# Optimization experiments

Measured on AMD Instinct MI355X. Metric: run time of the kernel, lower is better.

Reference implementation:

```python
import jax, jax.numpy as jnp
import numpy as np

B, H, W, C = 2, 192, 192, 192
WS, SHIFT, NH = 16, 8, 6


def _window_partition(x, ws):
    b, h, w, c = x.shape
    x = x.reshape(b, h // ws, ws, w // ws, ws, c)
    return x.transpose(0, 1, 3, 2, 4, 5).reshape(-1, ws, ws, c)


def _window_reverse(win, ws, h, w):
    b = win.shape[0] // ((h // ws) * (w // ws))
    x = win.reshape(b, h // ws, w // ws, ws, ws, -1)
    return x.transpose(0, 1, 3, 2, 4, 5).reshape(b, h, w, -1)


def _relative_position_index(ws):
    coords = np.stack(np.meshgrid(np.arange(ws), np.arange(ws), indexing="ij"))
    cf = coords.reshape(2, -1)
    rel = (cf[:, :, None] - cf[:, None, :]).transpose(1, 2, 0).astype(np.int64)
    rel[..., 0] += ws - 1
    rel[..., 1] += ws - 1
    rel[..., 0] *= 2 * ws - 1
    return rel.sum(-1)  # (ws*ws, ws*ws) in [0, (2ws-1)^2)


def _shift_attn_mask(h, w, ws, shift):
    img = np.zeros((1, h, w, 1), np.float32)
    cnt = 0
    for hs in (slice(0, -ws), slice(-ws, -shift), slice(-shift, None)):
        for wsl in (slice(0, -ws), slice(-ws, -shift), slice(-shift, None)):
            img[:, hs, wsl, :] = cnt
            cnt += 1
    mw = np.asarray(_window_partition(jnp.asarray(img), ws)).reshape(-1, ws * ws)
    diff = mw[:, None, :] - mw[:, :, None]
    return jnp.asarray(np.where(diff != 0, -100.0, 0.0).astype(np.float32))


def setup_inputs():
    key = jax.random.key(0)
    ks = jax.random.split(key, 4)
    x = jax.random.normal(ks[0], (B, H, W, C), jnp.float32)
    qkv = jax.random.normal(ks[1], (B, H, W, 3 * C), jnp.float32)
    rpb_table = 0.02 * jax.random.normal(ks[2], ((2 * WS - 1) ** 2, NH), jnp.float32)
    geo_scale = jnp.full((NH,), 0.01, jnp.float32)
    geo_sigma = jnp.asarray(1.0, jnp.float32)
    proj_w = 0.02 * jax.random.normal(ks[3], (C, C), jnp.float32)
    proj_b = jnp.zeros((C,), jnp.float32)
    rpi = jnp.asarray(_relative_position_index(WS), jnp.int32)
    attn_mask = _shift_attn_mask(H, W, WS, SHIFT)
    return dict(x=x, qkv=qkv, rpb_table=rpb_table, geo_scale=geo_scale,
                geo_sigma=geo_sigma, proj_w=proj_w, proj_b=proj_b,
                rpi=rpi, attn_mask=attn_mask,
                window_size=WS, shift_size=SHIFT, num_heads=NH)


def _geo_bias(f, ws, sigma):
    # f: (nwb, ws, ws, C). L-shaped geodesic path: horizontal then vertical cumsums.
    nwb = f.shape[0]
    diff_h = jnp.sum(jnp.abs(f[:, :, 1:] - f[:, :, :-1]), -1)  # (nwb, ws, ws-1)
    ct_h = jnp.cumsum(jnp.concatenate(
        [jnp.zeros((nwb, ws, 1), f.dtype), 1.0 + sigma * diff_h], -1), -1)
    diff_v = jnp.sum(jnp.abs(f[:, 1:] - f[:, :-1]), -1)        # (nwb, ws-1, ws)
    ct_v = jnp.cumsum(jnp.concatenate(
        [jnp.zeros((nwb, 1, ws), f.dtype), 1.0 + sigma * diff_v], -2), -2)
    idx = jnp.arange(ws * ws)
    rows, cols = idx // ws, idx % ws
    ct_h_flat = ct_h[:, rows, cols]                    # (nwb, n)
    ct_v_flat = ct_v[:, rows, cols]
    ct_h_corner = ct_h[:, rows[:, None], cols[None, :]]  # ct_h[ri, cj] -> (nwb, n, n)
    ct_v_corner = ct_v[:, rows[:, None], cols[None, :]]
    geo_h = jnp.abs(ct_h_corner - ct_h_flat[:, :, None])
    geo_v = jnp.abs(ct_v_flat[:, None, :] - ct_v_corner)
    return geo_h + geo_v                               # (nwb, n, n)


def _forward(x, qkv, rpb_table, geo_scale, geo_sigma, proj_w, proj_b,
             rpi, attn_mask, ws, shift, nh):
    b, h, w, c = x.shape
    n = ws * ws
    hd = c // nh
    sx = jnp.roll(x, (-shift, -shift), (1, 2))
    sqkv = jnp.roll(qkv, (-shift, -shift), (1, 2))
    f_win = _window_partition(sx, ws)                           # (nwb, ws, ws, c)
    geo = _geo_bias(f_win, ws, jnp.abs(geo_sigma))              # (nwb, n, n)
    qkv_win = _window_partition(sqkv, ws).reshape(-1, n, 3, nh, hd)
    q = qkv_win[:, :, 0].transpose(0, 2, 1, 3)                  # (nwb, nh, n, hd)
    k = qkv_win[:, :, 1].transpose(0, 2, 1, 3)
    v = qkv_win[:, :, 2].transpose(0, 2, 1, 3)
    attn = jnp.einsum("bhqd,bhkd->bhqk", q * (hd ** -0.5), k)   # (nwb, nh, n, n)
    rpb = rpb_table[rpi.reshape(-1)].reshape(n, n, nh).transpose(2, 0, 1)
    attn = attn + rpb[None]
    attn = attn - geo[:, None] * geo_scale[None, :, None, None]
    nw = attn_mask.shape[0]
    attn = attn.reshape(b, nw, nh, n, n) + attn_mask[None, :, None]
    attn = jax.nn.softmax(attn.reshape(-1, nh, n, n), axis=-1)
    out = jnp.einsum("bhqk,bhkd->bqhd", attn, v).reshape(-1, n, c)
    out = out @ proj_w.T + proj_b                               # nn.Linear
    out = _window_reverse(out.reshape(-1, ws, ws, c), ws, h, w)
    out = jnp.roll(out, (shift, shift), (1, 2))
    return out.reshape(b, h * w, c)


def reference(x, qkv, rpb_table, geo_scale, geo_sigma, proj_w, proj_b,
              rpi, attn_mask, window_size, shift_size, num_heads):
    return _forward(x, qkv, rpb_table, geo_scale, geo_sigma, proj_w, proj_b,
                    rpi, attn_mask, window_size, shift_size, num_heads)
```

## Files before the change

### kernel.cpp

```cpp
#include <hip/hip_runtime.h>
#include <stdint.h>

#define HH 192
#define WWW 192
#define CC 192
#define WS 16
#define SHIFTS 8
#define NH 6
#define HD 32
#define NN 256
#define NWS 12
#define NWIN_B 144
#define NWIN 288
#define CTN (NWIN * NN)

typedef _Float16 half_t;
typedef half_t half2_t __attribute__((ext_vector_type(2)));
typedef half_t f16x8 __attribute__((ext_vector_type(8)));
typedef float f32x4 __attribute__((ext_vector_type(4)));
typedef uint32_t u32x4 __attribute__((ext_vector_type(4)));

#define LOG2E 1.4426950408889634f

#if __has_builtin(__builtin_amdgcn_exp2f)
#define EXP2F(x) __builtin_amdgcn_exp2f(x)
#else
#define EXP2F(x) __expf(0.6931471805599453f * (x))
#endif

__device__ __forceinline__ float sat16(float a) {
    return fminf(fmaxf(a, -60000.f), 60000.f);
}
__device__ __forceinline__ uint32_t pack_h2(float a, float b) {
    half2_t h; h.x = (half_t)sat16(a); h.y = (half_t)sat16(b);
    return __builtin_bit_cast(uint32_t, h);
}
__device__ __forceinline__ uint32_t pack_p(float a, float b) {
    half2_t h; h.x = (half_t)a; h.y = (half_t)b;
    return __builtin_bit_cast(uint32_t, h);
}

__device__ __forceinline__ size_t xrow(int b, int sh, int sw) {
    int oh = sh + SHIFTS; if (oh >= HH) oh -= HH;
    int ow = sw + SHIFTS; if (ow >= WWW) ow -= WWW;
    return ((size_t)((b * HH + oh) * WWW + ow)) * CC;
}
__device__ __forceinline__ size_t qkvrow(int b, int sh, int sw) {
    int oh = sh + SHIFTS; if (oh >= HH) oh -= HH;
    int ow = sw + SHIFTS; if (ow >= WWW) ow -= WWW;
    return ((size_t)((b * HH + oh) * WWW + ow)) * (3 * CC);
}
__device__ __forceinline__ int regof(int v) { return v < (HH - WS) ? 0 : (v < (HH - SHIFTS) ? 1 : 2); }

__device__ __forceinline__ float* ctptr(float* o, int q) {
    int slot = q / 96;
    int off = q - slot * 96;
    return o + (size_t)slot * CC + 96 + off;
}

__global__ __launch_bounds__(256) void kgeo(const float* __restrict__ x,
                                            const float* __restrict__ sigp,
                                            float* __restrict__ outbuf) {
    __shared__ float dh[16][16];
    __shared__ float dv[16][16];
    int win = blockIdx.x;
    int b = win / NWIN_B, wi = win % NWIN_B;
    int wr = wi / NWS, wc = wi % NWS;
    int t = threadIdx.x;
    int r = t >> 4, j = t & 15;
    int r1 = (r < 15) ? r + 1 : r;
    int j1 = (j < 15) ? j + 1 : j;

    const float4* a4 = (const float4*)(x + xrow(b, wr * WS + r,  wc * WS + j));
    const float4* b4 = (const float4*)(x + xrow(b, wr * WS + r,  wc * WS + j1));
    const float4* c4 = (const float4*)(x + xrow(b, wr * WS + r1, wc * WS + j));
    float sh_ = 0.f, sv_ = 0.f;
    #pragma unroll 4
    for (int ch = 0; ch < 48; ch++) {
        float4 fa = a4[ch], fb = b4[ch], fc = c4[ch];
        sh_ += fabsf(fb.x - fa.x) + fabsf(fb.y - fa.y) + fabsf(fb.z - fa.z) + fabsf(fb.w - fa.w);
        sv_ += fabsf(fc.x - fa.x) + fabsf(fc.y - fa.y) + fabsf(fc.z - fa.z) + fabsf(fc.w - fa.w);
    }
    dh[r][j] = (j < 15) ? sh_ : 0.f;
    dv[r][j] = (r < 15) ? sv_ : 0.f;
    __syncthreads();

    float sigma = fabsf(sigp[0]);
    if (t < 16) {
        float acc = 0.f;
        *ctptr(outbuf, win * NN + t * 16) = 0.f;
        for (int jj = 1; jj < 16; jj++) {
            acc += 1.0f + sigma * dh[t][jj - 1];
            *ctptr(outbuf, win * NN + t * 16 + jj) = acc;
        }
    } else if (t < 32) {
        int c = t - 16;
        float acc = 0.f;
        *ctptr(outbuf, CTN + win * NN + c) = 0.f;
        for (int ii = 1; ii < 16; ii++) {
            acc += 1.0f + sigma * dv[ii - 1][c];
            *ctptr(outbuf, CTN + win * NN + ii * 16 + c) = acc;
        }
    }
}

__global__ __launch_bounds__(512, 4) void kattn(const float* __restrict__ qkv,
                                                const float* __restrict__ rpb_table,
                                                const float* __restrict__ geo_scale,
                                                float* __restrict__ outbuf) {
    __shared__ __align__(16) uint32_t Klds[256 * 20];
    __shared__ __align__(16) uint32_t Vt[32 * 140];
    __shared__ __align__(16) float cth_s[NN];
    __shared__ __align__(16) float ctv_s[NN];
    __shared__ float rpb_s[961];

    int win = blockIdx.x, head = blockIdx.y;
    int b = win / NWIN_B, wi = win % NWIN_B;
    int wr = wi / NWS, wc = wi % NWS;
    int wr16 = wr * WS, wc16 = wc * WS;
    int t = threadIdx.x;
    int dl = t & 15;
    int g = (t >> 4) & 3;
    int g4 = g * 4;
    int w = t >> 6;

    for (int i = t; i < 961; i += 512) rpb_s[i] = rpb_table[i * NH + head] * LOG2E;

    if (t < 256) {
        int r = t >> 4, c = t & 15;
        const float4* k4 = (const float4*)(qkv + qkvrow(b, wr16 + r, wc16 + c) + CC + head * HD);
        uint32_t kp[16];
        #pragma unroll
        for (int c4 = 0; c4 < 8; c4++) {
            float4 u = k4[c4];
            kp[c4 * 2 + 0] = pack_h2(u.x, u.y);
            kp[c4 * 2 + 1] = pack_h2(u.z, u.w);
        }
        uint4* dst = (uint4*)((char*)Klds + t * 80);
        #pragma unroll
        for (int i = 0; i < 4; i++)
            dst[i] = make_uint4(kp[i * 4 + 0], kp[i * 4 + 1], kp[i * 4 + 2], kp[i * 4 + 3]);
    } else if (t < 384) {
        int tv = t - 256;
        int p0 = 2 * tv, p1 = 2 * tv + 1;
        const float4* v0 = (const float4*)(qkv + qkvrow(b, wr16 + (p0 >> 4), wc16 + (p0 & 15)) + 2 * CC + head * HD);
        const float4* v1 = (const float4*)(qkv + qkvrow(b, wr16 + (p1 >> 4), wc16 + (p1 & 15)) + 2 * CC + head * HD);
        #pragma unroll
        for (int c4 = 0; c4 < 8; c4++) {
            float4 a = v0[c4], bu = v1[c4];
            Vt[(c4 * 4 + 0) * 140 + tv] = pack_h2(a.x, bu.x);
            Vt[(c4 * 4 + 1) * 140 + tv] = pack_h2(a.y, bu.y);
            Vt[(c4 * 4 + 2) * 140 + tv] = pack_h2(a.z, bu.z);
            Vt[(c4 * 4 + 3) * 140 + tv] = pack_h2(a.w, bu.w);
        }
    } else {
        int tc = t - 384;
        cth_s[tc]       = *ctptr(outbuf, win * NN + tc);
        cth_s[tc + 128] = *ctptr(outbuf, win * NN + tc + 128);
        ctv_s[tc]       = *ctptr(outbuf, CTN + win * NN + tc);
        ctv_s[tc + 128] = *ctptr(outbuf, CTN + win * NN + tc + 128);
    }
    f16x8 qf[2];
    #pragma unroll
    for (int qt = 0; qt < 2; qt++) {
        const float* qp = qkv + qkvrow(b, wr16 + 2 * w + qt, wc16 + dl) + head * HD + g * 8;
        float4 u0 = ((const float4*)qp)[0];
        float4 u1 = ((const float4*)qp)[1];
        f16x8 q8;
        q8[0] = (half_t)sat16(u0.x); q8[1] = (half_t)sat16(u0.y);
        q8[2] = (half_t)sat16(u0.z); q8[3] = (half_t)sat16(u0.w);
        q8[4] = (half_t)sat16(u1.x); q8[5] = (half_t)sat16(u1.y);
        q8[6] = (half_t)sat16(u1.z); q8[7] = (half_t)sat16(u1.w);
        qf[qt] = q8;
    }
    __syncthreads();

    float gscale2 = geo_scale[head] * LOG2E;
    float ghs[2][4];
    f32x4 Dv[2];
    int regq[2], qb0[2];
    #pragma unroll
    for (int qt = 0; qt < 2; qt++) {
        int rq = 2 * w + qt;
        float chq = cth_s[rq * 16 + dl];
        f32x4 Bv = *(const f32x4*)&cth_s[rq * 16 + g4];
        Dv[qt] = *(const f32x4*)&ctv_s[rq * 16 + g4];
        #pragma unroll
        for (int r = 0; r < 4; r++) ghs[qt][r] = -gscale2 * fabsf(Bv[r] - chq);
        regq[qt] = 3 * regof(wr16 + rq) + regof(wc16 + dl);
        qb0[qt] = rq * 31 + dl + 480 - g4;
    }
    int regkc[4];
    #pragma unroll
    for (int r = 0; r < 4; r++) regkc[r] = regof(wc16 + g4 + r);
    const float scale2 = 0.17677669529663687f * LOG2E;

    f32x4 o[2][2];
    #pragma unroll
    for (int qt = 0; qt < 2; qt++) { o[qt][0] = (f32x4){0.f,0.f,0.f,0.f}; o[qt][1] = (f32x4){0.f,0.f,0.f,0.f}; }
    float lq[2] = {0.f, 0.f};

    const char* KB = (const char*)Klds;
    const char* VB = (const char*)Vt;
    const f32x4 zf = {0.f, 0.f, 0.f, 0.f};
    int srcA = ((g & 1) << 5) + dl;
    int srcB = srcA + 16;
    bool hi = (g >= 2);

    #pragma unroll 2
    for (int kvb = 0; kvb < 8; kvb++) {
        int kv0 = kvb * 32;
        f16x8 ak0 = *(const f16x8*)(KB + (size_t)(kv0 + dl) * 80 + g * 16);
        f16x8 ak1 = *(const f16x8*)(KB + (size_t)(kv0 + 16 + dl) * 80 + g * 16);

        f32x4 s[2][2];
        #pragma unroll
        for (int qt = 0; qt < 2; qt++) {
            s[qt][0] = __builtin_amdgcn_mfma_f32_16x16x32_f16(ak0, qf[qt], zf, 0, 0, 0);
            s[qt][1] = __builtin_amdgcn_mfma_f32_16x16x32_f16(ak1, qf[qt], zf, 0, 0, 0);
        }

        f32x4 cv0 = *(const f32x4*)&ctv_s[kv0 + g4];
        f32x4 cv1 = *(const f32x4*)&ctv_s[kv0 + 16 + g4];
        int rowreg0 = 3 * regof(wr16 + kvb * 2);
        int rowreg1 = 3 * regof(wr16 + kvb * 2 + 1);

        uint32_t pkk[2][2][2];
        #pragma unroll
        for (int qt = 0; qt < 2; qt++) {
            #pragma unroll
            for (int kt = 0; kt < 2; kt++) {
                int rowreg = kt ? rowreg1 : rowreg0;
                int idxk = qb0[qt] - (kvb * 2 + kt) * 31;
                float pr[4];
                #pragma unroll
                for (int r = 0; r < 4; r++) {
                    float C = kt ? cv1[r] : cv0[r];
                    float geoV = fabsf(C - Dv[qt][r]);
                    float bias = rpb_s[idxk - r] + ghs[qt][r]
                               + ((rowreg + regkc[r] == regq[qt]) ? 0.f : -100.f * LOG2E);
                    float tt = fmaf(s[qt][kt][r], scale2, fmaf(-gscale2, geoV, bias));
                    tt = fminf(fmaxf(tt, -1000.f), 15.f);
                    float p = EXP2F(tt);
                    lq[qt] += p;
                    pr[r] = p;
                }
                pkk[qt][kt][0] = pack_p(pr[0], pr[1]);
                pkk[qt][kt][1] = pack_p(pr[2], pr[3]);
            }
        }

        f16x8 bv0 = *(const f16x8*)(VB + (size_t)dl * 560 + kv0 * 2 + g * 16);
        f16x8 bv1 = *(const f16x8*)(VB + (size_t)(16 + dl) * 560 + kv0 * 2 + g * 16);

        #pragma unroll
        for (int qt = 0; qt < 2; qt++) {
            uint32_t a00 = __shfl((int)pkk[qt][0][0], srcA), a01 = __shfl((int)pkk[qt][0][1], srcA);
            uint32_t a10 = __shfl((int)pkk[qt][0][0], srcB), a11 = __shfl((int)pkk[qt][0][1], srcB);
            uint32_t b00 = __shfl((int)pkk[qt][1][0], srcA), b01 = __shfl((int)pkk[qt][1][1], srcA);
            uint32_t b10 = __shfl((int)pkk[qt][1][0], srcB), b11 = __shfl((int)pkk[qt][1][1], srcB);
            u32x4 uu;
            uu.x = hi ? b00 : a00; uu.y = hi ? b01 : a01;
            uu.z = hi ? b10 : a10; uu.w = hi ? b11 : a11;
            f16x8 ap = __builtin_bit_cast(f16x8, uu);
            o[qt][0] = __builtin_amdgcn_mfma_f32_16x16x32_f16(ap, bv0, o[qt][0], 0, 0, 0);
            o[qt][1] = __builtin_amdgcn_mfma_f32_16x16x32_f16(ap, bv1, o[qt][1], 0, 0, 0);
        }
    }

    float invr[2][4];
    #pragma unroll
    for (int qt = 0; qt < 2; qt++) {
        float li = lq[qt];
        li += __shfl_xor(li, 16);
        li += __shfl_xor(li, 32);
        float iv = 1.0f / li;
        #pragma unroll
        for (int r = 0; r < 4; r++) invr[qt][r] = __shfl(iv, g4 + r);
    }

    __syncthreads();
    char* OB = (char*)Klds + w * 2560;
    #pragma unroll
    for (int qt = 0; qt < 2; qt++)
        #pragma unroll
        for (int dt = 0; dt < 2; dt++)
            #pragma unroll
            for (int r = 0; r < 4; r++) {
                float val = o[qt][dt][r] * invr[qt][r];
                *(half_t*)(OB + (qt * 16 + g4 + r) * 80 + (dt * 16 + dl) * 2) = (half_t)sat16(val);
            }

    int lane = t & 63;
    int lp = lane >> 1, half = lane & 1;
    int tok = 32 * w + lp;
    int rr = tok >> 4, pc = tok & 15;
    int oh = wr16 + rr + SHIFTS; if (oh >= HH) oh -= HH;
    int ow = wc16 + pc + SHIFTS; if (ow >= WWW) ow -= WWW;
    size_t R = (size_t)b * (HH * WWW) + (size_t)oh * WWW + ow;
    uint4* o4p = (uint4*)outbuf;
    const uint4* src = (const uint4*)(OB + lp * 80 + half * 32);
    size_t base4 = R * 48 + head * 4 + half * 2;
    o4p[base4 + 0] = src[0];
    o4p[base4 + 1] = src[1];
}

__global__ __launch_bounds__(512, 4) void kproj(float* __restrict__ data,
                                                const float* __restrict__ proj_w,
                                                const float* __restrict__ proj_b) {
    __shared__ __align__(16) uint32_t Wh[192 * 100];
    int t = threadIdx.x;
    size_t R0 = (size_t)blockIdx.x * 128;

    const float4* pw4 = (const float4*)proj_w;
    for (int q = t; q < 9216; q += 512) {
        int j = q / 48, c4 = q - j * 48;
        float4 u = pw4[q];
        *(uint2*)&Wh[j * 100 + c4 * 2] = make_uint2(pack_h2(u.x, u.y), pack_h2(u.z, u.w));
    }
    __syncthreads();

    int dl = t & 15, g = (t >> 4) & 3, w = t >> 6;
    const char* WB = (const char*)Wh;
    const char* AB = (const char*)data;

    f32x4 acc[12];
    #pragma unroll
    for (int i = 0; i < 12; i++) acc[i] = (f32x4){0.f, 0.f, 0.f, 0.f};

    size_t arow = (size_t)(R0 + w * 16 + dl) * 768;
    #pragma unroll
    for (int ch = 0; ch < 6; ch++) {
        f16x8 af = *(const f16x8*)(AB + arow + ch * 64 + g * 16);
        #pragma unroll
        for (int jt = 0; jt < 12; jt++) {
            f16x8 bf = *(const f16x8*)(WB + (size_t)(jt * 16 + dl) * 400 + ch * 64 + g * 16);
            acc[jt] = __builtin_amdgcn_mfma_f32_16x16x32_f16(af, bf, acc[jt], 0, 0, 0);
        }
    }

    float bvv[12];
    #pragma unroll
    for (int jt = 0; jt < 12; jt++) bvv[jt] = proj_b[jt * 16 + dl];
    size_t orow = (size_t)(R0 + w * 16 + g * 4) * 192;
    #pragma unroll
    for (int jt = 0; jt < 12; jt++)
        #pragma unroll
        for (int r = 0; r < 4; r++)
            data[orow + (size_t)r * 192 + jt * 16 + dl] = acc[jt][r] + bvv[jt];
}

extern "C" void kernel_launch(void* const* d_in, const int* in_sizes, int n_in,
                              void* d_out, int out_size, void* d_ws, size_t ws_size,
                              hipStream_t stream) {
    const float *x = nullptr, *qkv = nullptr, *rpb = nullptr, *gsc = nullptr,
                *pw = nullptr, *pb = nullptr, *sig = nullptr;
    for (int i = 0; i < n_in; i++) {
        switch (in_sizes[i]) {
            case 14155776: x   = (const float*)d_in[i]; break;
            case 42467328: qkv = (const float*)d_in[i]; break;
            case 5766:     rpb = (const float*)d_in[i]; break;
            case 6:        gsc = (const float*)d_in[i]; break;
            case 36864:    pw  = (const float*)d_in[i]; break;
            case 192:      pb  = (const float*)d_in[i]; break;
            default: break;
        }
    }
    if (n_in > 4 && in_sizes[4] == 1) sig = (const float*)d_in[4];
    else for (int i = 0; i < n_in; i++) if (in_sizes[i] == 1) { sig = (const float*)d_in[i]; break; }
    if (!x)   x   = (const float*)d_in[0];
    if (!qkv) qkv = (const float*)d_in[1];
    if (!rpb) rpb = (const float*)d_in[2];
    if (!gsc) gsc = (const float*)d_in[3];
    if (!sig) sig = (const float*)d_in[4];
    if (!pw)  pw  = (const float*)d_in[5];
    if (!pb)  pb  = (const float*)d_in[6];

    float* out = (float*)d_out;

    kgeo<<<dim3(NWIN), dim3(256), 0, stream>>>(x, sig, out);
    kattn<<<dim3(NWIN, NH), dim3(512), 0, stream>>>(qkv, rpb, gsc, out);
    kproj<<<dim3((NWIN * NN) / 128), dim3(512), 0, stream>>>(out, pw, pb);
}
```

Measured before the change: 406.9 us.

## Specialize attention loop for unmasked windows and vectorize relative-position bias reads

The attention kernel gets two copies of the inner KV loop: windows away from the shifted border skip the region-mask computation entirely, while border windows keep it. The relative position bias is pre-expanded in shared memory so each lane fetches its four bias values with one vector load instead of four scalar indexed reads. The geodesic-distance kernel also splits the channel reduction across two thread halves with 512 threads per block. The cost is larger code size from the duplicated loop and more shared memory for the expanded bias table, which could lower occupancy.

```diff
diff --git a/kernel.cpp b/kernel.cpp
--- a/kernel.cpp
+++ b/kernel.cpp
@@ -58,31 +58,32 @@
     return o + (size_t)slot * CC + 96 + off;
 }
 
-__global__ __launch_bounds__(256) void kgeo(const float* __restrict__ x,
+__global__ __launch_bounds__(512) void kgeo(const float* __restrict__ x,
                                             const float* __restrict__ sigp,
                                             float* __restrict__ outbuf) {
-    __shared__ float dh[16][16];
-    __shared__ float dv[16][16];
+    __shared__ float dh[2][16][16];
+    __shared__ float dv[2][16][16];
     int win = blockIdx.x;
     int b = win / NWIN_B, wi = win % NWIN_B;
     int wr = wi / NWS, wc = wi % NWS;
     int t = threadIdx.x;
-    int r = t >> 4, j = t & 15;
+    int hf = t >> 8, tt = t & 255;
+    int r = tt >> 4, j = tt & 15;
     int r1 = (r < 15) ? r + 1 : r;
     int j1 = (j < 15) ? j + 1 : j;
 
-    const float4* a4 = (const float4*)(x + xrow(b, wr * WS + r,  wc * WS + j));
-    const float4* b4 = (const float4*)(x + xrow(b, wr * WS + r,  wc * WS + j1));
-    const float4* c4 = (const float4*)(x + xrow(b, wr * WS + r1, wc * WS + j));
+    const float4* a4 = (const float4*)(x + xrow(b, wr * WS + r,  wc * WS + j))  + hf * 24;
+    const float4* b4 = (const float4*)(x + xrow(b, wr * WS + r,  wc * WS + j1)) + hf * 24;
+    const float4* c4 = (const float4*)(x + xrow(b, wr * WS + r1, wc * WS + j))  + hf * 24;
     float sh_ = 0.f, sv_ = 0.f;
     #pragma unroll 4
-    for (int ch = 0; ch < 48; ch++) {
+    for (int ch = 0; ch < 24; ch++) {
         float4 fa = a4[ch], fb = b4[ch], fc = c4[ch];
         sh_ += fabsf(fb.x - fa.x) + fabsf(fb.y - fa.y) + fabsf(fb.z - fa.z) + fabsf(fb.w - fa.w);
         sv_ += fabsf(fc.x - fa.x) + fabsf(fc.y - fa.y) + fabsf(fc.z - fa.z) + fabsf(fc.w - fa.w);
     }
-    dh[r][j] = (j < 15) ? sh_ : 0.f;
-    dv[r][j] = (r < 15) ? sv_ : 0.f;
+    dh[hf][r][j] = (j < 15) ? sh_ : 0.f;
+    dv[hf][r][j] = (r < 15) ? sv_ : 0.f;
     __syncthreads();
 
     float sigma = fabsf(sigp[0]);
@@ -90,7 +91,7 @@
         float acc = 0.f;
         *ctptr(outbuf, win * NN + t * 16) = 0.f;
         for (int jj = 1; jj < 16; jj++) {
-            acc += 1.0f + sigma * dh[t][jj - 1];
+            acc += 1.0f + sigma * (dh[0][t][jj - 1] + dh[1][t][jj - 1]);
             *ctptr(outbuf, win * NN + t * 16 + jj) = acc;
         }
     } else if (t < 32) {
@@ -98,7 +99,7 @@
         float acc = 0.f;
         *ctptr(outbuf, CTN + win * NN + c) = 0.f;
         for (int ii = 1; ii < 16; ii++) {
-            acc += 1.0f + sigma * dv[ii - 1][c];
+            acc += 1.0f + sigma * (dv[0][ii - 1][c] + dv[1][ii - 1][c]);
             *ctptr(outbuf, CTN + win * NN + ii * 16 + c) = acc;
         }
     }
@@ -112,7 +113,7 @@
     __shared__ __align__(16) uint32_t Vt[32 * 140];
     __shared__ __align__(16) float cth_s[NN];
     __shared__ __align__(16) float ctv_s[NN];
-    __shared__ float rpb_s[961];
+    __shared__ __align__(16) float rpbT[31 * 64 * 4];
 
     int win = blockIdx.x, head = blockIdx.y;
     int b = win / NWIN_B, wi = win % NWIN_B;
@@ -122,9 +123,21 @@
     int dl = t & 15;
     int g = (t >> 4) & 3;
     int g4 = g * 4;
+    int g16dl = g * 16 + dl;
     int w = t >> 6;
 
-    for (int i = t; i < 961; i += 512) rpb_s[i] = rpb_table[i * NH + head] * LOG2E;
+    for (int e = t; e < 31 * 64; e += 512) {
+        int u = e >> 6;
+        int l16 = e & 63;
+        int dd = l16 & 15, gg = l16 >> 4;
+        int base = u * 31 + dd - gg * 4 + 15;
+        float4 v;
+        v.x = rpb_table[(base    ) * NH + head] * LOG2E;
+        v.y = rpb_table[(base - 1) * NH + head] * LOG2E;
+        v.z = rpb_table[(base - 2) * NH + head] * LOG2E;
+        v.w = rpb_table[(base - 3) * NH + head] * LOG2E;
+        *(float4*)&rpbT[e * 4] = v;
+    }
 
     if (t < 256) {
         int r = t >> 4, c = t & 15;
@@ -178,7 +191,7 @@
     float gscale2 = geo_scale[head] * LOG2E;
     float ghs[2][4];
     f32x4 Dv[2];
-    int regq[2], qb0[2];
+    int regq[2];
     #pragma unroll
     for (int qt = 0; qt < 2; qt++) {
         int rq = 2 * w + qt;
@@ -188,7 +201,6 @@
         #pragma unroll
         for (int r = 0; r < 4; r++) ghs[qt][r] = -gscale2 * fabsf(Bv[r] - chq);
         regq[qt] = 3 * regof(wr16 + rq) + regof(wc16 + dl);
-        qb0[qt] = rq * 31 + dl + 480 - g4;
     }
     int regkc[4];
     #pragma unroll
@@ -207,66 +219,68 @@
     int srcB = srcA + 16;
     bool hi = (g >= 2);
 
-    #pragma unroll 2
-    for (int kvb = 0; kvb < 8; kvb++) {
-        int kv0 = kvb * 32;
-        f16x8 ak0 = *(const f16x8*)(KB + (size_t)(kv0 + dl) * 80 + g * 16);
-        f16x8 ak1 = *(const f16x8*)(KB + (size_t)(kv0 + 16 + dl) * 80 + g * 16);
-
-        f32x4 s[2][2];
-        #pragma unroll
-        for (int qt = 0; qt < 2; qt++) {
-            s[qt][0] = __builtin_amdgcn_mfma_f32_16x16x32_f16(ak0, qf[qt], zf, 0, 0, 0);
-            s[qt][1] = __builtin_amdgcn_mfma_f32_16x16x32_f16(ak1, qf[qt], zf, 0, 0, 0);
-        }
-
-        f32x4 cv0 = *(const f32x4*)&ctv_s[kv0 + g4];
-        f32x4 cv1 = *(const f32x4*)&ctv_s[kv0 + 16 + g4];
-        int rowreg0 = 3 * regof(wr16 + kvb * 2);
-        int rowreg1 = 3 * regof(wr16 + kvb * 2 + 1);
-
-        uint32_t pkk[2][2][2];
-        #pragma unroll
-        for (int qt = 0; qt < 2; qt++) {
-            #pragma unroll
-            for (int kt = 0; kt < 2; kt++) {
-                int rowreg = kt ? rowreg1 : rowreg0;
-                int idxk = qb0[qt] - (kvb * 2 + kt) * 31;
-                float pr[4];
-                #pragma unroll
-                for (int r = 0; r < 4; r++) {
-                    float C = kt ? cv1[r] : cv0[r];
-                    float geoV = fabsf(C - Dv[qt][r]);
-                    float bias = rpb_s[idxk - r] + ghs[qt][r]
-                               + ((rowreg + regkc[r] == regq[qt]) ? 0.f : -100.f * LOG2E);
-                    float tt = fmaf(s[qt][kt][r], scale2, fmaf(-gscale2, geoV, bias));
-                    tt = fminf(fmaxf(tt, -1000.f), 15.f);
-                    float p = EXP2F(tt);
-                    lq[qt] += p;
-                    pr[r] = p;
-                }
-                pkk[qt][kt][0] = pack_p(pr[0], pr[1]);
-                pkk[qt][kt][1] = pack_p(pr[2], pr[3]);
-            }
-        }
-
-        f16x8 bv0 = *(const f16x8*)(VB + (size_t)dl * 560 + kv0 * 2 + g * 16);
-        f16x8 bv1 = *(const f16x8*)(VB + (size_t)(16 + dl) * 560 + kv0 * 2 + g * 16);
-
-        #pragma unroll
-        for (int qt = 0; qt < 2; qt++) {
-            uint32_t a00 = __shfl((int)pkk[qt][0][0], srcA), a01 = __shfl((int)pkk[qt][0][1], srcA);
-            uint32_t a10 = __shfl((int)pkk[qt][0][0], srcB), a11 = __shfl((int)pkk[qt][0][1], srcB);
-            uint32_t b00 = __shfl((int)pkk[qt][1][0], srcA), b01 = __shfl((int)pkk[qt][1][1], srcA);
-            uint32_t b10 = __shfl((int)pkk[qt][1][0], srcB), b11 = __shfl((int)pkk[qt][1][1], srcB);
-            u32x4 uu;
-            uu.x = hi ? b00 : a00; uu.y = hi ? b01 : a01;
-            uu.z = hi ? b10 : a10; uu.w = hi ? b11 : a11;
-            f16x8 ap = __builtin_bit_cast(f16x8, uu);
-            o[qt][0] = __builtin_amdgcn_mfma_f32_16x16x32_f16(ap, bv0, o[qt][0], 0, 0, 0);
-            o[qt][1] = __builtin_amdgcn_mfma_f32_16x16x32_f16(ap, bv1, o[qt][1], 0, 0, 0);
-        }
-    }
+#define KVLOOP(MASKED)                                                                  \
+    _Pragma("unroll 2")                                                                 \
+    for (int kvb = 0; kvb < 8; kvb++) {                                                 \
+        int kv0 = kvb * 32;                                                             \
+        f16x8 ak0 = *(const f16x8*)(KB + (size_t)(kv0 + dl) * 80 + g * 16);             \
+        f16x8 ak1 = *(const f16x8*)(KB + (size_t)(kv0 + 16 + dl) * 80 + g * 16);        \
+        f32x4 s[2][2];                                                                  \
+        s[0][0] = __builtin_amdgcn_mfma_f32_16x16x32_f16(ak0, qf[0], zf, 0, 0, 0);      \
+        s[0][1] = __builtin_amdgcn_mfma_f32_16x16x32_f16(ak1, qf[0], zf, 0, 0, 0);      \
+        s[1][0] = __builtin_amdgcn_mfma_f32_16x16x32_f16(ak0, qf[1], zf, 0, 0, 0);      \
+        s[1][1] = __builtin_amdgcn_mfma_f32_16x16x32_f16(ak1, qf[1], zf, 0, 0, 0);      \
+        f32x4 cv0 = *(const f32x4*)&ctv_s[kv0 + g4];                                    \
+        f32x4 cv1 = *(const f32x4*)&ctv_s[kv0 + 16 + g4];                               \
+        uint32_t pkk[2][2][2];                                                          \
+        _Pragma("unroll")                                                               \
+        for (int qt = 0; qt < 2; qt++) {                                                \
+            _Pragma("unroll")                                                           \
+            for (int kt = 0; kt < 2; kt++) {                                            \
+                int rk = kvb * 2 + kt;                                                  \
+                f32x4 rv = *(const f32x4*)&rpbT[(size_t)((2 * w + qt - rk + 15) * 64 + g16dl) * 4]; \
+                int rowreg = MASKED ? 3 * regof(wr16 + rk) : 0;                         \
+                float pr[4];                                                            \
+                _Pragma("unroll")                                                       \
+                for (int r = 0; r < 4; r++) {                                           \
+                    float C = kt ? cv1[r] : cv0[r];                                     \
+                    float geoV = fabsf(C - Dv[qt][r]);                                  \
+                    float bias = rv[r] + ghs[qt][r];                                    \
+                    if (MASKED)                                                         \
+                        bias += ((rowreg + regkc[r] == regq[qt]) ? 0.f : -100.f * LOG2E); \
+                    float tt2 = fmaf(s[qt][kt][r], scale2, fmaf(-gscale2, geoV, bias)); \
+                    tt2 = fminf(fmaxf(tt2, -1000.f), 15.f);                             \
+                    float p = EXP2F(tt2);                                               \
+                    lq[qt] += p;                                                        \
+                    pr[r] = p;                                                          \
+                }                                                                       \
+                pkk[qt][kt][0] = pack_p(pr[0], pr[1]);                                  \
+                pkk[qt][kt][1] = pack_p(pr[2], pr[3]);                                  \
+            }                                                                           \
+        }                                                                               \
+        f16x8 bv0 = *(const f16x8*)(VB + (size_t)dl * 560 + kv0 * 2 + g * 16);          \
+        f16x8 bv1 = *(const f16x8*)(VB + (size_t)(16 + dl) * 560 + kv0 * 2 + g * 16);   \
+        _Pragma("unroll")                                                               \
+        for (int qt = 0; qt < 2; qt++) {                                                \
+            uint32_t a00 = __shfl((int)pkk[qt][0][0], srcA), a01 = __shfl((int)pkk[qt][0][1], srcA); \
+            uint32_t a10 = __shfl((int)pkk[qt][0][0], srcB), a11 = __shfl((int)pkk[qt][0][1], srcB); \
+            uint32_t b00 = __shfl((int)pkk[qt][1][0], srcA), b01 = __shfl((int)pkk[qt][1][1], srcA); \
+            uint32_t b10 = __shfl((int)pkk[qt][1][0], srcB), b11 = __shfl((int)pkk[qt][1][1], srcB); \
+            u32x4 uu;                                                                   \
+            uu.x = hi ? b00 : a00; uu.y = hi ? b01 : a01;                               \
+            uu.z = hi ? b10 : a10; uu.w = hi ? b11 : a11;                               \
+            f16x8 ap = __builtin_bit_cast(f16x8, uu);                                   \
+            o[qt][0] = __builtin_amdgcn_mfma_f32_16x16x32_f16(ap, bv0, o[qt][0], 0, 0, 0); \
+            o[qt][1] = __builtin_amdgcn_mfma_f32_16x16x32_f16(ap, bv1, o[qt][1], 0, 0, 0); \
+        }                                                                               \
+    }
+
+    if (wr < 11 && wc < 11) {
+        KVLOOP(false)
+    } else {
+        KVLOOP(true)
+    }
+#undef KVLOOP
 
     float invr[2][4];
     #pragma unroll
@@ -378,7 +392,7 @@
 
     float* out = (float*)d_out;
 
-    kgeo<<<dim3(NWIN), dim3(256), 0, stream>>>(x, sig, out);
+    kgeo<<<dim3(NWIN), dim3(512), 0, stream>>>(x, sig, out);
     kattn<<<dim3(NWIN, NH), dim3(512), 0, stream>>>(qkv, rpb, gsc, out);
     kproj<<<dim3((NWIN * NN) / 128), dim3(512), 0, stream>>>(out, pw, pb);
 }
```

New measurement: 411.4 us. No clear change (+1.1%).
